# Kernel tuning notes

Hardware: AMD Instinct MI355X
Metric: run time of the kernel (lower is better)

The kernel has to match this reference:

```python
import jax, jax.numpy as jnp
import numpy as np

B, T, D = 2, 2048, 1024
HEADS = 16
MEM = 512
HEAD_DIM = D // HEADS


def setup_inputs() -> dict:
    key = jax.random.key(0)
    k1, k2, k3, k4, k5 = jax.random.split(key, 5)
    x = jax.random.normal(k1, (B, T, D), dtype=jnp.float32)
    w_qkv = jax.random.normal(k2, (3 * D, D), dtype=jnp.float32) * (1.0 / np.sqrt(D))
    w_out = jax.random.normal(k3, (D, D), dtype=jnp.float32) * (1.0 / np.sqrt(D))
    b_out = jax.random.normal(k4, (D,), dtype=jnp.float32) * 0.01
    memory = jax.random.normal(k5, (MEM, D), dtype=jnp.float32)
    return {"x": x, "w_qkv": w_qkv, "w_out": w_out, "b_out": b_out, "memory": memory}


def reference(x, w_qkv, w_out, b_out, memory):
    b, t, d = x.shape
    h, hd = HEADS, HEAD_DIM
    scale = hd ** -0.5
    # QKV projection: [B,T,3D]
    qkv = jnp.einsum('btd,ed->bte', x, w_qkv)
    q, k, v = jnp.split(qkv, 3, axis=-1)
    # [B,H,T,hd]
    q = q.reshape(b, t, h, hd).transpose(0, 2, 1, 3)
    k = k.reshape(b, t, h, hd).transpose(0, 2, 1, 3)
    v = v.reshape(b, t, h, hd).transpose(0, 2, 1, 3)
    # memory K/V: [B,H,MEM,hd] (broadcast over batch)
    mem = memory.reshape(1, MEM, h, hd).transpose(0, 2, 1, 3)
    mem = jnp.broadcast_to(mem, (b, h, MEM, hd))
    k = jnp.concatenate([mem, k], axis=2)
    v = jnp.concatenate([mem, v], axis=2)
    # attention: scores [B,H,T,MEM+T]
    scores = jnp.einsum('bhqd,bhkd->bhqk', q, k) * scale
    weights = jax.nn.softmax(scores, axis=-1)
    out = jnp.einsum('bhqk,bhkd->bhqd', weights, v)
    out = out.transpose(0, 2, 1, 3).reshape(b, t, d)
    return jnp.einsum('btd,ed->bte', out, w_out) + b_out
```

## Files before the change

kernel.cpp:

```cpp
#include <hip/hip_runtime.h>
#include <hip/hip_bf16.h>
#include <stdint.h>

#define B_   2
#define T_   2048
#define D_   1024
#define H_   16
#define HD_  64
#define MEM_ 512
#define KV_  (MEM_ + T_)
#define NIT_ (KV_ / 64)

using bf16 = __bf16;
typedef __bf16 bf16x8 __attribute__((ext_vector_type(8)));
typedef float  f32x4  __attribute__((ext_vector_type(4)));
typedef short  s16x4  __attribute__((ext_vector_type(4)));

__device__ __forceinline__ f32x4 mfma16(bf16x8 a, bf16x8 b, f32x4 c) {
  return __builtin_amdgcn_mfma_f32_16x16x32_bf16(a, b, c, 0, 0, 0);
}
__device__ __forceinline__ f32x4 mfma16k16(s16x4 a, s16x4 b, f32x4 c) {
  return __builtin_amdgcn_mfma_f32_16x16x16bf16_1k(a, b, c, 0, 0, 0);
}

template <bool F32>
__device__ __forceinline__ bf16x8 load8(const void* p, size_t off) {
  if constexpr (F32) {
    const float* q = (const float*)p + off;
    f32x4 u = *(const f32x4*)q;
    f32x4 v = *(const f32x4*)(q + 4);
    bf16x8 r;
    r[0] = (bf16)u[0]; r[1] = (bf16)u[1]; r[2] = (bf16)u[2]; r[3] = (bf16)u[3];
    r[4] = (bf16)v[0]; r[5] = (bf16)v[1]; r[6] = (bf16)v[2]; r[7] = (bf16)v[3];
    return r;
  } else {
    return *(const bf16x8*)((const bf16*)p + off);
  }
}

__device__ __forceinline__ unsigned short bf16_bits(float f) {
  bf16 h = (bf16)f;
  return __builtin_bit_cast(unsigned short, h);
}

__device__ __forceinline__ ushort4 pack4(f32x4 v) {
  ushort4 p;
  p.x = bf16_bits(v[0]); p.y = bf16_bits(v[1]);
  p.z = bf16_bits(v[2]); p.w = bf16_bits(v[3]);
  return p;
}

__global__ void fill_mem(const float* __restrict__ memory,
                         bf16* __restrict__ mem_k, bf16* __restrict__ mem_vt) {
  int idx = blockIdx.x * 256 + threadIdx.x;
  int m = idx >> 10, d = idx & 1023;
  bf16 v = (bf16)memory[idx];
  mem_k[idx] = v;
  mem_vt[(size_t)d * MEM_ + m] = v;
}

template <int EPI, bool AF32, bool WF32, bool APLANE>
__global__ __launch_bounds__(256) void gemm_bt(
    const void* __restrict__ A, const void* __restrict__ W,
    const float* __restrict__ bias,
    bf16* __restrict__ q_ws, bf16* __restrict__ k_ws, bf16* __restrict__ vt_ws,
    float* __restrict__ Cout, int K) {
  __shared__ __align__(16) bf16 Als[128 * 32];
  __shared__ __align__(16) bf16 Bls[128 * 32];
  const int m0 = blockIdx.y * 128;
  const int n0 = blockIdx.x * 128;
  const int tid = threadIdx.x;
  const int w = tid >> 6;
  const int lane = tid & 63;
  const int lx = lane & 15;
  const int quad = lane >> 4;
  const int amb = (w & 1) * 64;
  const int bnb = (w >> 1) * 64;
  const int r0 = tid >> 2, seg = tid & 3;

  f32x4 acc[4][4];
#pragma unroll
  for (int i = 0; i < 4; i++)
#pragma unroll
    for (int j = 0; j < 4; j++) acc[i][j] = (f32x4){0.f, 0.f, 0.f, 0.f};

  for (int k0 = 0; k0 < K; k0 += 32) {
    bf16x8 a0, a1;
    if constexpr (APLANE) {
      int c0 = k0 + seg * 8, h = c0 >> 6, hd = c0 & 63;
      int mA = m0 + r0, mB = m0 + 64 + r0;
      a0 = load8<false>(A,
          ((size_t)((mA >> 11) * H_ + h) * T_ + (mA & 2047)) * HD_ + hd);
      a1 = load8<false>(A,
          ((size_t)((mB >> 11) * H_ + h) * T_ + (mB & 2047)) * HD_ + hd);
    } else {
      a0 = load8<AF32>(A, (size_t)(m0 + r0) * K + k0 + seg * 8);
      a1 = load8<AF32>(A, (size_t)(m0 + 64 + r0) * K + k0 + seg * 8);
    }
    bf16x8 b0 = load8<WF32>(W, (size_t)(n0 + r0) * K + k0 + seg * 8);
    bf16x8 b1 = load8<WF32>(W, (size_t)(n0 + 64 + r0) * K + k0 + seg * 8);
    __syncthreads();
    *(bf16x8*)&Als[tid * 8] = a0;
    *(bf16x8*)&Als[2048 + tid * 8] = a1;
    *(bf16x8*)&Bls[tid * 8] = b0;
    *(bf16x8*)&Bls[2048 + tid * 8] = b1;
    __syncthreads();

    bf16x8 af[4], bfr[4];
#pragma unroll
    for (int mt = 0; mt < 4; mt++)
      af[mt] = *(const bf16x8*)&Als[(amb + mt * 16 + lx) * 32 + quad * 8];
#pragma unroll
    for (int nt = 0; nt < 4; nt++)
      bfr[nt] = *(const bf16x8*)&Bls[(bnb + nt * 16 + lx) * 32 + quad * 8];
#pragma unroll
    for (int mt = 0; mt < 4; mt++)
#pragma unroll
      for (int nt = 0; nt < 4; nt++)
        acc[mt][nt] = mfma16(af[mt], bfr[nt], acc[mt][nt]);
  }

  if (EPI == 0) {
#pragma unroll
    for (int mt = 0; mt < 4; mt++) {
      int mbase = m0 + amb + mt * 16 + quad * 4;
      int b = mbase >> 11;
      int t = mbase & 2047;
#pragma unroll
      for (int nt = 0; nt < 4; nt++) {
        int col = n0 + bnb + nt * 16 + lx;
        int which = col >> 10;
        int d = col & 1023;
        int h = d >> 6, hdi = d & 63;
        int bh = b * H_ + h;
        if (which == 0) {
#pragma unroll
          for (int r = 0; r < 4; r++)
            q_ws[((size_t)bh * T_ + t + r) * HD_ + hdi] = (bf16)acc[mt][nt][r];
        } else if (which == 1) {
#pragma unroll
          for (int r = 0; r < 4; r++)
            k_ws[((size_t)bh * T_ + t + r) * HD_ + hdi] = (bf16)acc[mt][nt][r];
        } else {
          *(ushort4*)&vt_ws[((size_t)bh * HD_ + hdi) * T_ + t] =
              pack4(acc[mt][nt]);
        }
      }
    }
  } else {
#pragma unroll
    for (int nt = 0; nt < 4; nt++) {
      int col = n0 + bnb + nt * 16 + lx;
      float bias_f = bias[col];
#pragma unroll
      for (int mt = 0; mt < 4; mt++) {
        int mbase = m0 + amb + mt * 16 + quad * 4;
#pragma unroll
        for (int r = 0; r < 4; r++)
          Cout[(size_t)(mbase + r) * D_ + col] = acc[mt][nt][r] + bias_f;
      }
    }
  }
}

__global__ __launch_bounds__(256, 2) void attn_kernel(
    bf16* __restrict__ q_ws, const bf16* __restrict__ k_ws,
    const bf16* __restrict__ vt_ws, const bf16* __restrict__ mem_k,
    const bf16* __restrict__ mem_vt) {
  __shared__ __align__(16) bf16 Kls[64][72];
  __shared__ __align__(16) bf16 Vls[64][72];
  const int tid = threadIdx.x;
  const int w = tid >> 6;
  const int lane = tid & 63;
  const int lx = lane & 15;
  const int quad = lane >> 4;
  const int bh = blockIdx.x & 31;
  const int qt = blockIdx.x >> 5;
  const int q0 = qt * 128 + w * 32;
  const int h = bh & 15;

  const int srow1 = tid >> 3, soff1 = (tid & 7) * 8;
  const int srow2 = (tid + 256) >> 3, soff2 = soff1;

  bf16* qbase = q_ws + ((size_t)bh * T_ + q0) * HD_;

  const float QSCALE = 0.125f * 1.44269504089f;
  bf16x8 qf[2][2];
#pragma unroll
  for (int qg = 0; qg < 2; qg++)
#pragma unroll
    for (int hf = 0; hf < 2; hf++) {
      bf16x8 v = *(const bf16x8*)(qbase + (size_t)(qg * 16 + lx) * HD_ +
                                  hf * 32 + quad * 8);
#pragma unroll
      for (int i = 0; i < 8; i++)
        v[i] = (bf16)((float)v[i] * QSCALE);
      qf[qg][hf] = v;
    }

  const bf16* kplane = k_ws + (size_t)bh * T_ * HD_;
  const bf16* vtplane = vt_ws + (size_t)bh * HD_ * T_;
  const bf16* mkh = mem_k + h * HD_;
  const bf16* mvh = mem_vt + (size_t)h * HD_ * MEM_;

  f32x4 o[4][2];
#pragma unroll
  for (int mt = 0; mt < 4; mt++)
#pragma unroll
    for (int qg = 0; qg < 2; qg++) o[mt][qg] = (f32x4){0.f, 0.f, 0.f, 0.f};
  float lsum[2] = {0.f, 0.f};

  for (int it = 0; it < NIT_; it++) {
    const int kv0 = it * 64;
    const bool memPart = kv0 < MEM_;
    bf16x8 kr1, kr2, vr1, vr2;
    if (memPart) {
      kr1 = *(const bf16x8*)(mkh + (size_t)(kv0 + srow1) * D_ + soff1);
      kr2 = *(const bf16x8*)(mkh + (size_t)(kv0 + srow2) * D_ + soff2);
      vr1 = *(const bf16x8*)(mvh + (size_t)srow1 * MEM_ + kv0 + soff1);
      vr2 = *(const bf16x8*)(mvh + (size_t)srow2 * MEM_ + kv0 + soff2);
    } else {
      const int t0 = kv0 - MEM_;
      kr1 = *(const bf16x8*)(kplane + (size_t)(t0 + srow1) * HD_ + soff1);
      kr2 = *(const bf16x8*)(kplane + (size_t)(t0 + srow2) * HD_ + soff2);
      vr1 = *(const bf16x8*)(vtplane + (size_t)srow1 * T_ + t0 + soff1);
      vr2 = *(const bf16x8*)(vtplane + (size_t)srow2 * T_ + t0 + soff2);
    }
    __syncthreads();
    *(bf16x8*)&Kls[srow1][soff1] = kr1;
    *(bf16x8*)&Kls[srow2][soff2] = kr2;
    *(bf16x8*)&Vls[srow1][soff1] = vr1;
    *(bf16x8*)&Vls[srow2][soff2] = vr2;
    __syncthreads();

    f32x4 s[4][2];
#pragma unroll
    for (int g = 0; g < 4; g++) {
      bf16x8 ka0 = *(const bf16x8*)&Kls[g * 16 + lx][quad * 8];
      bf16x8 ka1 = *(const bf16x8*)&Kls[g * 16 + lx][32 + quad * 8];
#pragma unroll
      for (int qg = 0; qg < 2; qg++) {
        s[g][qg] = (f32x4){0.f, 0.f, 0.f, 0.f};
        s[g][qg] = mfma16(ka0, qf[qg][0], s[g][qg]);
        s[g][qg] = mfma16(ka1, qf[qg][1], s[g][qg]);
      }
    }

    s16x4 pb[2][4];
#pragma unroll
    for (int qg = 0; qg < 2; qg++) {
      float ps = 0.f;
#pragma unroll
      for (int g = 0; g < 4; g++) {
#pragma unroll
        for (int r = 0; r < 4; r++) {
          float p = __builtin_amdgcn_exp2f(s[g][qg][r]);
          ps += p;
          pb[qg][g][r] = (short)bf16_bits(p);
        }
      }
      lsum[qg] += ps;
    }

#pragma unroll
    for (int mt = 0; mt < 4; mt++) {
#pragma unroll
      for (int kk = 0; kk < 4; kk++) {
        s16x4 va = *(const s16x4*)&Vls[mt * 16 + lx][kk * 16 + quad * 4];
#pragma unroll
        for (int qg = 0; qg < 2; qg++)
          o[mt][qg] = mfma16k16(va, pb[qg][kk], o[mt][qg]);
      }
    }
  }

  float inv[2];
#pragma unroll
  for (int qg = 0; qg < 2; qg++) {
    float s2 = lsum[qg];
    s2 += __shfl_xor(s2, 16);
    s2 += __shfl_xor(s2, 32);
    inv[qg] = 1.f / s2;
  }

#pragma unroll
  for (int qg = 0; qg < 2; qg++) {
#pragma unroll
    for (int mt = 0; mt < 4; mt++) {
      f32x4 ov;
#pragma unroll
      for (int r = 0; r < 4; r++) ov[r] = o[mt][qg][r] * inv[qg];
      *(ushort4*)(qbase + (size_t)(qg * 16 + lx) * HD_ + mt * 16 + quad * 4)
          = pack4(ov);
    }
  }
}

extern "C" void kernel_launch(void* const* d_in, const int* in_sizes, int n_in,
                              void* d_out, int out_size, void* d_ws,
                              size_t ws_size, hipStream_t stream) {
  const void*  x      = d_in[0];
  const void*  w_qkv  = d_in[1];
  const void*  w_out  = d_in[2];
  const float* b_out  = (const float*)d_in[3];
  const float* memory = (const float*)d_in[4];

  char* ws = (char*)d_ws;
  bf16* q_ws   = (bf16*)(ws);
  bf16* k_ws   = (bf16*)(ws + (8u << 20));
  bf16* vt_ws  = (bf16*)(ws + (16u << 20));
  bf16* mem_k  = (bf16*)(ws + (24u << 20));
  bf16* mem_vt = (bf16*)(ws + (25u << 20));
  float* out = (float*)d_out;

  fill_mem<<<dim3(2048), dim3(256), 0, stream>>>(memory, mem_k, mem_vt);
  gemm_bt<0, true, true, false><<<dim3(24, 32), dim3(256), 0, stream>>>(
      x, w_qkv, nullptr, q_ws, k_ws, vt_ws, nullptr, 1024);
  attn_kernel<<<dim3(512), dim3(256), 0, stream>>>(
      q_ws, k_ws, vt_ws, mem_k, mem_vt);
  gemm_bt<1, false, true, true><<<dim3(8, 32), dim3(256), 0, stream>>>(
      q_ws, w_out, b_out, nullptr, nullptr, nullptr, out, 1024);
}
```

Measured before the change: 223.3 us.

## Pre-convert inputs to bf16 and stage tiles via direct global-to-LDS loads with swizzle

Adds conversion kernels that turn x, w_qkv and w_out into bf16 scratch copies before the GEMMs, so those GEMMs read bf16 instead of converting fp32 in the inner loop. Both the GEMM and attention kernels now fill shared memory with global_load_lds 16-byte loads that bypass registers, using XOR-swizzled layouts in place of padded arrays to avoid bank conflicts. Memory K is re-laid out per head so its rows are contiguous. The extra conversion launches add memory traffic, and the output buffer and workspace are reused as scratch space for the converted copies.

After: 222.3 us. Within noise of the previous version (-0.4%).

```diff
diff --git a/kernel.cpp b/kernel.cpp
--- a/kernel.cpp
+++ b/kernel.cpp
@@ -23,19 +23,10 @@
   return __builtin_amdgcn_mfma_f32_16x16x16bf16_1k(a, b, c, 0, 0, 0);
 }
 
-template <bool F32>
-__device__ __forceinline__ bf16x8 load8(const void* p, size_t off) {
-  if constexpr (F32) {
-    const float* q = (const float*)p + off;
-    f32x4 u = *(const f32x4*)q;
-    f32x4 v = *(const f32x4*)(q + 4);
-    bf16x8 r;
-    r[0] = (bf16)u[0]; r[1] = (bf16)u[1]; r[2] = (bf16)u[2]; r[3] = (bf16)u[3];
-    r[4] = (bf16)v[0]; r[5] = (bf16)v[1]; r[6] = (bf16)v[2]; r[7] = (bf16)v[3];
-    return r;
-  } else {
-    return *(const bf16x8*)((const bf16*)p + off);
-  }
+__device__ __forceinline__ void gll16(const void* g, void* l) {
+  __builtin_amdgcn_global_load_lds(
+      (const __attribute__((address_space(1))) unsigned int*)g,
+      (__attribute__((address_space(3))) unsigned int*)l, 16, 0, 0);
 }
 
 __device__ __forceinline__ unsigned short bf16_bits(float f) {
@@ -50,23 +41,36 @@
   return p;
 }
 
+__global__ void conv_bf16(const float* __restrict__ s, bf16* __restrict__ d) {
+  size_t i = ((size_t)blockIdx.x * 256 + threadIdx.x) * 8;
+  f32x4 a = *(const f32x4*)(s + i);
+  f32x4 b = *(const f32x4*)(s + i + 4);
+  bf16x8 r;
+  r[0] = (bf16)a[0]; r[1] = (bf16)a[1]; r[2] = (bf16)a[2]; r[3] = (bf16)a[3];
+  r[4] = (bf16)b[0]; r[5] = (bf16)b[1]; r[6] = (bf16)b[2]; r[7] = (bf16)b[3];
+  *(bf16x8*)(d + i) = r;
+}
+
 __global__ void fill_mem(const float* __restrict__ memory,
                          bf16* __restrict__ mem_k, bf16* __restrict__ mem_vt) {
   int idx = blockIdx.x * 256 + threadIdx.x;
   int m = idx >> 10, d = idx & 1023;
+  int hh = d >> 6, hd = d & 63;
   bf16 v = (bf16)memory[idx];
-  mem_k[idx] = v;
+  mem_k[((size_t)hh * MEM_ + m) * HD_ + hd] = v;
   mem_vt[(size_t)d * MEM_ + m] = v;
 }
 
-template <int EPI, bool AF32, bool WF32, bool APLANE>
+template <int EPI, bool APLANE>
 __global__ __launch_bounds__(256) void gemm_bt(
-    const void* __restrict__ A, const void* __restrict__ W,
+    const bf16* __restrict__ A, const bf16* __restrict__ W,
     const float* __restrict__ bias,
     bf16* __restrict__ q_ws, bf16* __restrict__ k_ws, bf16* __restrict__ vt_ws,
     float* __restrict__ Cout, int K) {
   __shared__ __align__(16) bf16 Als[128 * 32];
   __shared__ __align__(16) bf16 Bls[128 * 32];
+  char* AB = (char*)Als;
+  char* BB = (char*)Bls;
   const int m0 = blockIdx.y * 128;
   const int n0 = blockIdx.x * 128;
   const int tid = threadIdx.x;
@@ -76,7 +80,9 @@
   const int quad = lane >> 4;
   const int amb = (w & 1) * 64;
   const int bnb = (w >> 1) * 64;
-  const int r0 = tid >> 2, seg = tid & 3;
+  const int r0 = tid >> 2;
+  const int cs = (tid & 3) ^ ((tid >> 3) & 3);
+  const int rsw = (lx >> 1) & 3;
 
   f32x4 acc[4][4];
 #pragma unroll
@@ -85,34 +91,35 @@
     for (int j = 0; j < 4; j++) acc[i][j] = (f32x4){0.f, 0.f, 0.f, 0.f};
 
   for (int k0 = 0; k0 < K; k0 += 32) {
-    bf16x8 a0, a1;
+    const bf16 *pa0, *pa1;
     if constexpr (APLANE) {
-      int c0 = k0 + seg * 8, h = c0 >> 6, hd = c0 & 63;
-      int mA = m0 + r0, mB = m0 + 64 + r0;
-      a0 = load8<false>(A,
-          ((size_t)((mA >> 11) * H_ + h) * T_ + (mA & 2047)) * HD_ + hd);
-      a1 = load8<false>(A,
-          ((size_t)((mB >> 11) * H_ + h) * T_ + (mB & 2047)) * HD_ + hd);
+      int c0 = k0 + cs * 8, hh = c0 >> 6, hd = c0 & 63;
+      int mA = m0 + r0, mB = mA + 64;
+      pa0 = A + ((size_t)((mA >> 11) * H_ + hh) * T_ + (mA & 2047)) * HD_ + hd;
+      pa1 = A + ((size_t)((mB >> 11) * H_ + hh) * T_ + (mB & 2047)) * HD_ + hd;
     } else {
-      a0 = load8<AF32>(A, (size_t)(m0 + r0) * K + k0 + seg * 8);
-      a1 = load8<AF32>(A, (size_t)(m0 + 64 + r0) * K + k0 + seg * 8);
-    }
-    bf16x8 b0 = load8<WF32>(W, (size_t)(n0 + r0) * K + k0 + seg * 8);
-    bf16x8 b1 = load8<WF32>(W, (size_t)(n0 + 64 + r0) * K + k0 + seg * 8);
+      pa0 = A + (size_t)(m0 + r0) * K + k0 + cs * 8;
+      pa1 = pa0 + (size_t)64 * K;
+    }
+    const bf16* pb0 = W + (size_t)(n0 + r0) * K + k0 + cs * 8;
+    const bf16* pb1 = pb0 + (size_t)64 * K;
+
     __syncthreads();
-    *(bf16x8*)&Als[tid * 8] = a0;
-    *(bf16x8*)&Als[2048 + tid * 8] = a1;
-    *(bf16x8*)&Bls[tid * 8] = b0;
-    *(bf16x8*)&Bls[2048 + tid * 8] = b1;
+    gll16(pa0, AB + tid * 16);
+    gll16(pa1, AB + tid * 16 + 4096);
+    gll16(pb0, BB + tid * 16);
+    gll16(pb1, BB + tid * 16 + 4096);
     __syncthreads();
 
     bf16x8 af[4], bfr[4];
 #pragma unroll
     for (int mt = 0; mt < 4; mt++)
-      af[mt] = *(const bf16x8*)&Als[(amb + mt * 16 + lx) * 32 + quad * 8];
+      af[mt] = *(const bf16x8*)(AB + (size_t)(amb + mt * 16 + lx) * 64 +
+                                ((quad ^ rsw) * 16));
 #pragma unroll
     for (int nt = 0; nt < 4; nt++)
-      bfr[nt] = *(const bf16x8*)&Bls[(bnb + nt * 16 + lx) * 32 + quad * 8];
+      bfr[nt] = *(const bf16x8*)(BB + (size_t)(bnb + nt * 16 + lx) * 64 +
+                                 ((quad ^ rsw) * 16));
 #pragma unroll
     for (int mt = 0; mt < 4; mt++)
 #pragma unroll
@@ -131,8 +138,8 @@
         int col = n0 + bnb + nt * 16 + lx;
         int which = col >> 10;
         int d = col & 1023;
-        int h = d >> 6, hdi = d & 63;
-        int bh = b * H_ + h;
+        int hh = d >> 6, hdi = d & 63;
+        int bh = b * H_ + hh;
         if (which == 0) {
 #pragma unroll
           for (int r = 0; r < 4; r++)
@@ -167,8 +174,10 @@
     bf16* __restrict__ q_ws, const bf16* __restrict__ k_ws,
     const bf16* __restrict__ vt_ws, const bf16* __restrict__ mem_k,
     const bf16* __restrict__ mem_vt) {
-  __shared__ __align__(16) bf16 Kls[64][72];
-  __shared__ __align__(16) bf16 Vls[64][72];
+  __shared__ __align__(16) bf16 Kls[64 * 64];
+  __shared__ __align__(16) bf16 Vls[64 * 64];
+  char* KB = (char*)Kls;
+  char* VB = (char*)Vls;
   const int tid = threadIdx.x;
   const int w = tid >> 6;
   const int lane = tid & 63;
@@ -179,8 +188,8 @@
   const int q0 = qt * 128 + w * 32;
   const int h = bh & 15;
 
-  const int srow1 = tid >> 3, soff1 = (tid & 7) * 8;
-  const int srow2 = (tid + 256) >> 3, soff2 = soff1;
+  const int srow1 = tid >> 3;
+  const int sc1 = (tid & 7) ^ (srow1 & 7);
 
   bf16* qbase = q_ws + ((size_t)bh * T_ + q0) * HD_;
 
@@ -198,10 +207,10 @@
       qf[qg][hf] = v;
     }
 
-  const bf16* kplane = k_ws + (size_t)bh * T_ * HD_;
-  const bf16* vtplane = vt_ws + (size_t)bh * HD_ * T_;
-  const bf16* mkh = mem_k + h * HD_;
-  const bf16* mvh = mem_vt + (size_t)h * HD_ * MEM_;
+  const bf16* kpl = k_ws + (size_t)bh * T_ * HD_;
+  const bf16* vpl = vt_ws + (size_t)bh * HD_ * T_;
+  const bf16* mkp = mem_k + (size_t)h * MEM_ * HD_;
+  const bf16* mvp = mem_vt + (size_t)h * HD_ * MEM_;
 
   f32x4 o[4][2];
 #pragma unroll
@@ -212,32 +221,33 @@
 
   for (int it = 0; it < NIT_; it++) {
     const int kv0 = it * 64;
-    const bool memPart = kv0 < MEM_;
-    bf16x8 kr1, kr2, vr1, vr2;
-    if (memPart) {
-      kr1 = *(const bf16x8*)(mkh + (size_t)(kv0 + srow1) * D_ + soff1);
-      kr2 = *(const bf16x8*)(mkh + (size_t)(kv0 + srow2) * D_ + soff2);
-      vr1 = *(const bf16x8*)(mvh + (size_t)srow1 * MEM_ + kv0 + soff1);
-      vr2 = *(const bf16x8*)(mvh + (size_t)srow2 * MEM_ + kv0 + soff2);
+    const bf16 *kp1, *kp2, *vp1, *vp2;
+    if (kv0 < MEM_) {
+      kp1 = mkp + (size_t)(kv0 + srow1) * HD_ + sc1 * 8;
+      kp2 = kp1 + (size_t)32 * HD_;
+      vp1 = mvp + (size_t)srow1 * MEM_ + kv0 + sc1 * 8;
+      vp2 = vp1 + (size_t)32 * MEM_;
     } else {
       const int t0 = kv0 - MEM_;
-      kr1 = *(const bf16x8*)(kplane + (size_t)(t0 + srow1) * HD_ + soff1);
-      kr2 = *(const bf16x8*)(kplane + (size_t)(t0 + srow2) * HD_ + soff2);
-      vr1 = *(const bf16x8*)(vtplane + (size_t)srow1 * T_ + t0 + soff1);
-      vr2 = *(const bf16x8*)(vtplane + (size_t)srow2 * T_ + t0 + soff2);
+      kp1 = kpl + (size_t)(t0 + srow1) * HD_ + sc1 * 8;
+      kp2 = kp1 + (size_t)32 * HD_;
+      vp1 = vpl + (size_t)srow1 * T_ + t0 + sc1 * 8;
+      vp2 = vp1 + (size_t)32 * T_;
     }
     __syncthreads();
-    *(bf16x8*)&Kls[srow1][soff1] = kr1;
-    *(bf16x8*)&Kls[srow2][soff2] = kr2;
-    *(bf16x8*)&Vls[srow1][soff1] = vr1;
-    *(bf16x8*)&Vls[srow2][soff2] = vr2;
+    gll16(kp1, KB + tid * 16);
+    gll16(kp2, KB + tid * 16 + 4096);
+    gll16(vp1, VB + tid * 16);
+    gll16(vp2, VB + tid * 16 + 4096);
     __syncthreads();
 
+    const int sw = (lx & 7) << 4;
     f32x4 s[4][2];
 #pragma unroll
     for (int g = 0; g < 4; g++) {
-      bf16x8 ka0 = *(const bf16x8*)&Kls[g * 16 + lx][quad * 8];
-      bf16x8 ka1 = *(const bf16x8*)&Kls[g * 16 + lx][32 + quad * 8];
+      const char* kb = KB + (size_t)(g * 16 + lx) * 128;
+      bf16x8 ka0 = *(const bf16x8*)(kb + ((quad * 16) ^ sw));
+      bf16x8 ka1 = *(const bf16x8*)(kb + ((64 + quad * 16) ^ sw));
 #pragma unroll
       for (int qg = 0; qg < 2; qg++) {
         s[g][qg] = (f32x4){0.f, 0.f, 0.f, 0.f};
@@ -264,9 +274,10 @@
 
 #pragma unroll
     for (int mt = 0; mt < 4; mt++) {
+      const char* vb = VB + (size_t)(mt * 16 + lx) * 128;
 #pragma unroll
       for (int kk = 0; kk < 4; kk++) {
-        s16x4 va = *(const s16x4*)&Vls[mt * 16 + lx][kk * 16 + quad * 4];
+        s16x4 va = *(const s16x4*)(vb + ((kk * 32 + quad * 8) ^ sw));
 #pragma unroll
         for (int qg = 0; qg < 2; qg++)
           o[mt][qg] = mfma16k16(va, pb[qg][kk], o[mt][qg]);
@@ -299,9 +310,9 @@
 extern "C" void kernel_launch(void* const* d_in, const int* in_sizes, int n_in,
                               void* d_out, int out_size, void* d_ws,
                               size_t ws_size, hipStream_t stream) {
-  const void*  x      = d_in[0];
-  const void*  w_qkv  = d_in[1];
-  const void*  w_out  = d_in[2];
+  const float* x      = (const float*)d_in[0];
+  const float* w_qkv  = (const float*)d_in[1];
+  const float* w_out  = (const float*)d_in[2];
   const float* b_out  = (const float*)d_in[3];
   const float* memory = (const float*)d_in[4];
 
@@ -313,11 +324,19 @@
   bf16* mem_vt = (bf16*)(ws + (25u << 20));
   float* out = (float*)d_out;
 
+  char* outc = (char*)d_out;
+  bf16* xb  = (bf16*)(outc);
+  bf16* wqb = (bf16*)(outc + (8u << 20));
+  bf16* wob = (bf16*)(ws + (8u << 20));
+
+  conv_bf16<<<dim3(2048), dim3(256), 0, stream>>>(x, xb);
+  conv_bf16<<<dim3(1536), dim3(256), 0, stream>>>(w_qkv, wqb);
   fill_mem<<<dim3(2048), dim3(256), 0, stream>>>(memory, mem_k, mem_vt);
-  gemm_bt<0, true, true, false><<<dim3(24, 32), dim3(256), 0, stream>>>(
-      x, w_qkv, nullptr, q_ws, k_ws, vt_ws, nullptr, 1024);
+  gemm_bt<0, false><<<dim3(24, 32), dim3(256), 0, stream>>>(
+      xb, wqb, nullptr, q_ws, k_ws, vt_ws, nullptr, 1024);
   attn_kernel<<<dim3(512), dim3(256), 0, stream>>>(
       q_ws, k_ws, vt_ws, mem_k, mem_vt);
-  gemm_bt<1, false, true, true><<<dim3(8, 32), dim3(256), 0, stream>>>(
-      q_ws, w_out, b_out, nullptr, nullptr, nullptr, out, 1024);
-}
+  conv_bf16<<<dim3(512), dim3(256), 0, stream>>>(w_out, wob);
+  gemm_bt<1, true><<<dim3(8, 32), dim3(256), 0, stream>>>(
+      q_ws, wob, b_out, nullptr, nullptr, nullptr, out, 1024);
+}
```
